# Kernel optimization log

Measured on AMD Instinct MI355X. Metric: run time of the kernel, lower is better.

## Reference

```python
import jax, jax.numpy as jnp
import numpy as np

D_MODEL, WIN, STRIDE, NHEAD, HEAD_DIM, FFN_H = 96, 16, 8, 6, 16, 192
INNER = NHEAD * HEAD_DIM
EPS = 1e-5


def _ln(x, g, b):
    m = jnp.mean(x, axis=-1, keepdims=True)
    v = jnp.mean((x - m) ** 2, axis=-1, keepdims=True)
    return (x - m) / jnp.sqrt(v + EPS) * g + b


def setup_inputs() -> dict:
    key = jax.random.key(0)
    ks = jax.random.split(key, 16)
    B, L, D = 32, 8192, D_MODEL
    sd = lambda n: 1.0 / np.sqrt(n)
    return {
        "x": jax.random.normal(ks[0], (B, L, D), jnp.float32),
        "ln1_g": jnp.ones((D,), jnp.float32),
        "ln1_b": jnp.zeros((D,), jnp.float32),
        "qkv_w": jax.random.normal(ks[1], (D, 3 * INNER), jnp.float32) * sd(D),
        "qkv_b": jnp.zeros((3 * INNER,), jnp.float32),
        "out_w": jax.random.normal(ks[2], (INNER, D), jnp.float32) * sd(INNER),
        "out_b": jnp.zeros((D,), jnp.float32),
        "ln2_g": jnp.ones((D,), jnp.float32),
        "ln2_b": jnp.zeros((D,), jnp.float32),
        "ffn_w1": jax.random.normal(ks[3], (D, FFN_H), jnp.float32) * sd(D),
        "ffn_b1": jnp.zeros((FFN_H,), jnp.float32),
        "ffn_w2": jax.random.normal(ks[4], (FFN_H, D), jnp.float32) * sd(FFN_H),
        "ffn_b2": jnp.zeros((D,), jnp.float32),
        "pln_g": jnp.ones((D,), jnp.float32),
        "pln_b": jnp.zeros((D,), jnp.float32),
    }


def reference(x, ln1_g, ln1_b, qkv_w, qkv_b, out_w, out_b,
              ln2_g, ln2_b, ffn_w1, ffn_b1, ffn_w2, ffn_b2, pln_g, pln_b):
    B, L, D = x.shape
    w, s = WIN, STRIDE
    num_win = 1 + (L - w) // s  # all windows fit since (num_win-1)*s + w <= L
    idx = jnp.arange(num_win)[:, None] * s + jnp.arange(w)[None, :]  # [N, w]

    seg = x[:, idx]  # [B, N, w, D] gather of overlapping windows

    # --- pre-LN attention block, vectorized over all windows ---
    h = _ln(seg, ln1_g, ln1_b)
    qkv = h @ qkv_w + qkv_b  # [B, N, w, 3*INNER]
    q, k, v = jnp.split(qkv, 3, axis=-1)
    shp = (B, num_win, w, NHEAD, HEAD_DIM)
    q, k, v = q.reshape(shp), k.reshape(shp), v.reshape(shp)
    scores = jnp.einsum('bnqhd,bnkhd->bnhqk', q, k) / np.sqrt(HEAD_DIM).astype(np.float32)
    causal = jnp.tril(jnp.ones((w, w), bool))
    scores = jnp.where(causal, scores, -jnp.inf)
    attn = jax.nn.softmax(scores, axis=-1)
    o = jnp.einsum('bnhqk,bnkhd->bnqhd', attn, v).reshape(B, num_win, w, INNER)
    o = o @ out_w + out_b
    h = seg + o

    # --- FFN block ---
    h2 = _ln(h, ln2_g, ln2_b)
    h = h + (jax.nn.gelu(h2 @ ffn_w1 + ffn_b1) @ ffn_w2 + ffn_b2)
    h = _ln(h, pln_g, pln_b)

    # --- overlap-add average ---
    out = jnp.zeros((B, L, D), x.dtype).at[:, idx].add(h)
    cnt = jnp.zeros((L,), x.dtype).at[idx.reshape(-1)].add(1.0)
    return out / jnp.maximum(cnt, 1.0)[None, :, None]
```

## Files before the change

### kernel.cpp

```cpp
#include <hip/hip_runtime.h>
#include <hip/hip_bf16.h>

typedef __attribute__((ext_vector_type(8))) short short8;
typedef __attribute__((ext_vector_type(4))) float f32x4;
typedef __attribute__((ext_vector_type(4))) unsigned u32x4;

#define LDS_BYTES 40960
#define SH   104
#define SU   52
#define KOFF 3328
#define VOFF 6656
#define F1S  200
#define F1SU 100

#if __has_builtin(__builtin_amdgcn_cvt_pk_bf16_f32)
typedef __attribute__((ext_vector_type(2))) __bf16 bf16x2;
__device__ __forceinline__ unsigned pk2bf(float a, float b){
  bf16x2 v = __builtin_amdgcn_cvt_pk_bf16_f32(a, b);
  return __builtin_bit_cast(unsigned, v);
}
__device__ __forceinline__ unsigned short f2bf(float x){
  bf16x2 v = __builtin_amdgcn_cvt_pk_bf16_f32(x, x);
  return (unsigned short)(__builtin_bit_cast(unsigned, v) & 0xFFFFu);
}
#else
__device__ __forceinline__ unsigned short f2bf(float x){
  unsigned u = __float_as_uint(x);
  u += 0x7FFFu + ((u >> 16) & 1u);
  return (unsigned short)(u >> 16);
}
__device__ __forceinline__ unsigned pk2bf(float a, float b){
  return (unsigned)f2bf(a) | ((unsigned)f2bf(b) << 16);
}
#endif

#if __has_builtin(__builtin_amdgcn_rcpf)
__device__ __forceinline__ float fast_rcp(float x){ return __builtin_amdgcn_rcpf(x); }
#else
__device__ __forceinline__ float fast_rcp(float x){ return 1.f/x; }
#endif
#if __has_builtin(__builtin_amdgcn_rsqf)
__device__ __forceinline__ float fast_rsq(float x){ return __builtin_amdgcn_rsqf(x); }
#else
__device__ __forceinline__ float fast_rsq(float x){ return rsqrtf(x); }
#endif
#if __has_builtin(__builtin_amdgcn_exp2f)
__device__ __forceinline__ float fast_ex2(float x){ return __builtin_amdgcn_exp2f(x); }
#else
__device__ __forceinline__ float fast_ex2(float x){ return exp2f(x); }
#endif

__device__ __forceinline__ float bflo(unsigned u){ return __uint_as_float(u << 16); }
__device__ __forceinline__ float bfhi(unsigned u){ return __uint_as_float(u & 0xFFFF0000u); }
__device__ __forceinline__ float bf1(unsigned short h){ return __uint_as_float(((unsigned)h) << 16); }

__global__ void zero_stripes(float* __restrict__ out){
  int k = blockIdx.x;
  int b = blockIdx.y;
  int t = threadIdx.x;
  int tok = 24*k + (t / 24);
  f32x4 z = {0.f, 0.f, 0.f, 0.f};
  *(f32x4*)(out + ((size_t)b*8192 + tok)*96 + 4*(t % 24)) = z;
}

__global__ void pack_weights(const float* __restrict__ qkv_w, const float* __restrict__ out_w,
                             const float* __restrict__ ffn_w1, const float* __restrict__ ffn_w2,
                             short8* __restrict__ wsv){
  int f = blockIdx.x, lane = threadIdx.x;
  const float* W; int N, nt, kf;
  if (f < 54)      { W = qkv_w;  N = 288; nt = f/3;        kf = f%3; }
  else if (f < 72) { int i=f-54;  W = out_w;  N = 96;  nt = i/3; kf = i%3; }
  else if (f < 108){ int i=f-72;  W = ffn_w1; N = 192; nt = i/3; kf = i%3; }
  else             { int i=f-108; W = ffn_w2; N = 96;  nt = i/6; kf = i%6; }
  int n = lane & 15, kq = lane >> 4;
  short8 v;
#pragma unroll
  for (int j = 0; j < 8; ++j){
    int k = kf*32 + kq*8 + j;
    v[j] = (short)f2bf(W[(size_t)k * N + nt*16 + n]);
  }
  wsv[f*64 + lane] = v;
}

__global__ __launch_bounds__(512, 8)
void fused_block(const float* __restrict__ x,
                 const float* __restrict__ ln1_g, const float* __restrict__ ln1_b,
                 const float* __restrict__ qkv_b,
                 const float* __restrict__ out_b,
                 const float* __restrict__ ln2_g, const float* __restrict__ ln2_b,
                 const float* __restrict__ ffn_b1, const float* __restrict__ ffn_b2,
                 const float* __restrict__ pln_g, const float* __restrict__ pln_b,
                 const short8* __restrict__ wsv,
                 float* __restrict__ out)
{
  __shared__ __align__(16) char smem[LDS_BYTES];
  unsigned short* hres  = (unsigned short*)smem;
  unsigned*       hresU = (unsigned*)smem;
  unsigned short* buf1  = (unsigned short*)(smem + 9984);
  unsigned*       buf1U = (unsigned*)(smem + 9984);
  unsigned short* buf2  = (unsigned short*)(smem + 19968);
  unsigned*       buf2U = (unsigned*)(smem + 19968);

  const int tid  = threadIdx.x;
  const int wave = tid >> 6, lane = tid & 63;
  const int lm   = lane & 15, quad = lane >> 4;
  __builtin_assume(wave >= 0 && wave < 8);
  __builtin_assume(lm >= 0 && lm < 16);
  __builtin_assume(quad >= 0 && quad < 4);
  const int g = blockIdx.x, b = blockIdx.y;
  const int t0 = 24 * g;
  const size_t xbase = ((size_t)b * 8192 + t0) * 96;
  const short8* wl = wsv + lane;

  {
    const int row = tid >> 4, j = tid & 15;
    const float* xr = x + xbase + (size_t)row*96 + 6*j;
    float v[6];
#pragma unroll
    for (int e = 0; e < 3; ++e){ float2 t = *(const float2*)(xr + 2*e); v[2*e]=t.x; v[2*e+1]=t.y; }
    float s = 0.f, q2 = 0.f;
#pragma unroll
    for (int e = 0; e < 6; ++e){ s += v[e]; q2 += v[e]*v[e]; }
#pragma unroll
    for (int m = 1; m < 16; m <<= 1){ s += __shfl_xor(s, m, 16); q2 += __shfl_xor(q2, m, 16); }
    float mean = s * (1.f/96.f);
    float rstd = fast_rsq(q2 * (1.f/96.f) - mean*mean + 1e-5f);
#pragma unroll
    for (int e = 0; e < 3; ++e){
      float2 gg = *(const float2*)(ln1_g + 6*j + 2*e);
      float2 bb = *(const float2*)(ln1_b + 6*j + 2*e);
      buf1U[row*SU + 3*j + e] = pk2bf((v[2*e]-mean)*rstd*gg.x+bb.x,
                                      (v[2*e+1]-mean)*rstd*gg.y+bb.y);
    }
  }
  __syncthreads();

  {
    const int mt = wave & 1, p = wave >> 1;
    __builtin_assume(p >= 0 && p < 4);
    const unsigned short* arow = buf1 + (16*mt + lm)*SH + quad*8;
    short8 h0 = *(const short8*)(arow);
    short8 h1 = *(const short8*)(arow + 32);
    short8 h2 = *(const short8*)(arow + 64);
    auto qkv_tile = [&](int nt){
      if (nt < 12){
        f32x4 acc0 = *(const f32x4*)(qkv_b + nt*16 + quad*4);
        f32x4 acc1 = {0.f,0.f,0.f,0.f};
        acc0 = __builtin_amdgcn_mfma_f32_16x16x32_bf16(wl[(nt*3+0)*64], h0, acc0, 0, 0, 0);
        acc1 = __builtin_amdgcn_mfma_f32_16x16x32_bf16(wl[(nt*3+1)*64], h1, acc1, 0, 0, 0);
        acc0 = __builtin_amdgcn_mfma_f32_16x16x32_bf16(wl[(nt*3+2)*64], h2, acc0, 0, 0, 0);
        int row = 16*mt + lm;
        unsigned idx = (nt < 6)
          ? (unsigned)(row*SU + nt*8 + quad*2)
          : (unsigned)((KOFF>>1) + row*SU + (nt-6)*8 + quad*2);
        buf2U[idx]     = pk2bf(acc0[0]+acc1[0], acc0[1]+acc1[1]);
        buf2U[idx + 1] = pk2bf(acc0[2]+acc1[2], acc0[3]+acc1[3]);
      } else {
        int col = nt*16 + lm;
        float bias = qkv_b[col];
        f32x4 acc0 = {bias, bias, bias, bias};
        f32x4 acc1 = {0.f,0.f,0.f,0.f};
        acc0 = __builtin_amdgcn_mfma_f32_16x16x32_bf16(h0, wl[(nt*3+0)*64], acc0, 0, 0, 0);
        acc1 = __builtin_amdgcn_mfma_f32_16x16x32_bf16(h1, wl[(nt*3+1)*64], acc1, 0, 0, 0);
        acc0 = __builtin_amdgcn_mfma_f32_16x16x32_bf16(h2, wl[(nt*3+2)*64], acc0, 0, 0, 0);
        int d2 = col - 192;
        int w0 = (VOFF >> 1) + d2*20 + 8*mt + 2*quad;
        buf2U[w0]     = pk2bf(acc0[0]+acc1[0], acc0[1]+acc1[1]);
        buf2U[w0 + 1] = pk2bf(acc0[2]+acc1[2], acc0[3]+acc1[3]);
      }
    };
#pragma unroll
    for (int i = 0; i < 4; ++i) qkv_tile(p + 4*i);
    if (p < 2) qkv_tile(p + 16);
  }
  __syncthreads();

  {
    const short8 z8 = {0,0,0,0,0,0,0,0};
    short8 qa0=z8,ka0=z8,va0=z8, qa1=z8,ka1=z8,va1=z8, qa2=z8,ka2=z8,va2=z8;
    const int u0 = wave, u1 = wave + 8, u2 = wave + 16;
    const int w0_=u0/6, h0_=u0-6*(u0/6), w1_=u1/6, h1_=u1-6*(u1/6);
    const int w2_=u2/6, h2_=u2-6*(u2/6);
    if (quad < 2){
      qa0 = *(const short8*)(buf2 +        (8*w0_ + lm)*SH + h0_*16 + quad*8);
      ka0 = *(const short8*)(buf2 + KOFF + (8*w0_ + lm)*SH + h0_*16 + quad*8);
      va0 = *(const short8*)(buf2 + VOFF + (h0_*16 + lm)*40 + 8*w0_ + quad*8);
      qa1 = *(const short8*)(buf2 +        (8*w1_ + lm)*SH + h1_*16 + quad*8);
      ka1 = *(const short8*)(buf2 + KOFF + (8*w1_ + lm)*SH + h1_*16 + quad*8);
      va1 = *(const short8*)(buf2 + VOFF + (h1_*16 + lm)*40 + 8*w1_ + quad*8);
      if (wave < 2){
        qa2 = *(const short8*)(buf2 +        (8*w2_ + lm)*SH + h2_*16 + quad*8);
        ka2 = *(const short8*)(buf2 + KOFF + (8*w2_ + lm)*SH + h2_*16 + quad*8);
        va2 = *(const short8*)(buf2 + VOFF + (h2_*16 + lm)*40 + 8*w2_ + quad*8);
      }
    }
    auto attn_compute = [&](short8 qa, short8 ka, short8 va, int w, int h){
      f32x4 sc = {0.f,0.f,0.f,0.f};
      sc = __builtin_amdgcn_mfma_f32_16x16x32_bf16(ka, qa, sc, 0, 0, 0);
      float p4[4]; float sum = 0.f;
#pragma unroll
      for (int r = 0; r < 4; ++r){
        int k = quad*4 + r;
        float e = fast_ex2(sc[r]*0.36067376f);
        p4[r] = (k <= lm) ? e : 0.f;
        sum += p4[r];
      }
      sum += __shfl_xor(sum, 16);
      sum += __shfl_xor(sum, 32);
      float rs = fast_rcp(sum);
      int x0 = (int)pk2bf(p4[0]*rs, p4[1]*rs);
      int x1 = (int)pk2bf(p4[2]*rs, p4[3]*rs);
      int srcA = lm + ((quad & 1) << 5);
      int e0 = __shfl(x0, srcA),      e1 = __shfl(x1, srcA);
      int e2 = __shfl(x0, srcA + 16), e3 = __shfl(x1, srcA + 16);
      short8 pa = z8;
      if (quad < 2){
        u32x4 t = {(unsigned)e0, (unsigned)e1, (unsigned)e2, (unsigned)e3};
        pa = __builtin_bit_cast(short8, t);
      }
      f32x4 oc = {0.f,0.f,0.f,0.f};
      oc = __builtin_amdgcn_mfma_f32_16x16x32_bf16(va, pa, oc, 0, 0, 0);
      unsigned ob = (w*16 + lm)*SU + h*8 + quad*2;
      buf1U[ob]     = pk2bf(oc[0], oc[1]);
      buf1U[ob + 1] = pk2bf(oc[2], oc[3]);
    };
    attn_compute(qa0, ka0, va0, w0_, h0_);
    attn_compute(qa1, ka1, va1, w1_, h1_);
    if (wave < 2) attn_compute(qa2, ka2, va2, w2_, h2_);
  }
  __syncthreads();

  if (wave < 6){
    const int w = wave >> 1, ntb = (wave & 1)*3;
    const unsigned short* arow = buf1 + (w*16 + lm)*SH + quad*8;
    short8 a0 = *(const short8*)(arow);
    short8 a1 = *(const short8*)(arow + 32);
    short8 a2 = *(const short8*)(arow + 64);
    f32x4 xr[3];
#pragma unroll
    for (int i = 0; i < 3; ++i)
      xr[i] = *(const f32x4*)(x + xbase + (size_t)(8*w + lm)*96 + (ntb+i)*16 + quad*4);
#pragma unroll
    for (int i = 0; i < 3; ++i){
      int nt = ntb + i;
      f32x4 acc0 = *(const f32x4*)(out_b + nt*16 + quad*4);
      f32x4 acc1 = {0.f,0.f,0.f,0.f};
      acc0 = __builtin_amdgcn_mfma_f32_16x16x32_bf16(wl[(54 + nt*3 + 0)*64], a0, acc0, 0, 0, 0);
      acc1 = __builtin_amdgcn_mfma_f32_16x16x32_bf16(wl[(54 + nt*3 + 1)*64], a1, acc1, 0, 0, 0);
      acc0 = __builtin_amdgcn_mfma_f32_16x16x32_bf16(wl[(54 + nt*3 + 2)*64], a2, acc0, 0, 0, 0);
      unsigned idx = (w*16 + lm)*SU + nt*8 + quad*2;
      hresU[idx]     = pk2bf(acc0[0]+acc1[0]+xr[i][0], acc0[1]+acc1[1]+xr[i][1]);
      hresU[idx + 1] = pk2bf(acc0[2]+acc1[2]+xr[i][2], acc0[3]+acc1[3]+xr[i][3]);
    }
  }
  __syncthreads();

  {
    const int j = tid & 15;
#pragma unroll
    for (int p = 0; p < 2; ++p){
      int row = p*32 + (tid >> 4);
      if (row < 48){
        float v[6];
#pragma unroll
        for (int e = 0; e < 3; ++e){
          unsigned u = hresU[row*SU + 3*j + e];
          v[2*e] = bflo(u); v[2*e+1] = bfhi(u);
        }
        float s = 0.f, q2 = 0.f;
#pragma unroll
        for (int e = 0; e < 6; ++e){ s += v[e]; q2 += v[e]*v[e]; }
#pragma unroll
        for (int m = 1; m < 16; m <<= 1){ s += __shfl_xor(s, m, 16); q2 += __shfl_xor(q2, m, 16); }
        float mean = s * (1.f/96.f);
        float rstd = fast_rsq(q2 * (1.f/96.f) - mean*mean + 1e-5f);
#pragma unroll
        for (int e = 0; e < 3; ++e){
          float2 gg = *(const float2*)(ln2_g + 6*j + 2*e);
          float2 bb = *(const float2*)(ln2_b + 6*j + 2*e);
          buf1U[row*SU + 3*j + e] = pk2bf((v[2*e]-mean)*rstd*gg.x+bb.x,
                                          (v[2*e+1]-mean)*rstd*gg.y+bb.y);
        }
      }
    }
  }
  __syncthreads();

  if (wave < 6){
    const int mt = wave >> 1, ntb = (wave & 1)*6;
    const unsigned short* arow = buf1 + (mt*16 + lm)*SH + quad*8;
    short8 a0 = *(const short8*)(arow);
    short8 a1 = *(const short8*)(arow + 32);
    short8 a2 = *(const short8*)(arow + 64);
#pragma unroll
    for (int i = 0; i < 6; ++i){
      int nt = ntb + i;
      f32x4 acc0 = *(const f32x4*)(ffn_b1 + nt*16 + quad*4);
      f32x4 acc1 = {0.f,0.f,0.f,0.f};
      acc0 = __builtin_amdgcn_mfma_f32_16x16x32_bf16(wl[(72 + nt*3 + 0)*64], a0, acc0, 0, 0, 0);
      acc1 = __builtin_amdgcn_mfma_f32_16x16x32_bf16(wl[(72 + nt*3 + 1)*64], a1, acc1, 0, 0, 0);
      acc0 = __builtin_amdgcn_mfma_f32_16x16x32_bf16(wl[(72 + nt*3 + 2)*64], a2, acc0, 0, 0, 0);
      float gl[4];
#pragma unroll
      for (int r = 0; r < 4; ++r){
        float uu = acc0[r] + acc1[r];
        float z = -2.3022081f * (uu + 0.044715f * uu*uu*uu);
        float e = fast_ex2(z);
        gl[r] = uu * fast_rcp(1.f + e);
      }
      unsigned idx = (mt*16 + lm)*F1SU + nt*8 + quad*2;
      buf2U[idx]     = pk2bf(gl[0], gl[1]);
      buf2U[idx + 1] = pk2bf(gl[2], gl[3]);
    }
  }
  __syncthreads();

  if (wave < 6){
    const int mt = wave >> 1, ntb = (wave & 1)*3;
    const unsigned short* frow = buf2 + (mt*16 + lm)*F1S + quad*8;
    short8 f0 = *(const short8*)(frow);
    short8 f1 = *(const short8*)(frow + 32);
    short8 f2 = *(const short8*)(frow + 64);
    short8 f3 = *(const short8*)(frow + 96);
    short8 f4 = *(const short8*)(frow + 128);
    short8 f5 = *(const short8*)(frow + 160);
#pragma unroll
    for (int i = 0; i < 3; ++i){
      int nt = ntb + i;
      f32x4 acc0 = *(const f32x4*)(ffn_b2 + nt*16 + quad*4);
      f32x4 acc1 = {0.f,0.f,0.f,0.f};
      acc0 = __builtin_amdgcn_mfma_f32_16x16x32_bf16(wl[(108 + nt*6 + 0)*64], f0, acc0, 0, 0, 0);
      acc1 = __builtin_amdgcn_mfma_f32_16x16x32_bf16(wl[(108 + nt*6 + 1)*64], f1, acc1, 0, 0, 0);
      acc0 = __builtin_amdgcn_mfma_f32_16x16x32_bf16(wl[(108 + nt*6 + 2)*64], f2, acc0, 0, 0, 0);
      acc1 = __builtin_amdgcn_mfma_f32_16x16x32_bf16(wl[(108 + nt*6 + 3)*64], f3, acc1, 0, 0, 0);
      acc0 = __builtin_amdgcn_mfma_f32_16x16x32_bf16(wl[(108 + nt*6 + 4)*64], f4, acc0, 0, 0, 0);
      acc1 = __builtin_amdgcn_mfma_f32_16x16x32_bf16(wl[(108 + nt*6 + 5)*64], f5, acc1, 0, 0, 0);
      unsigned idx = (mt*16 + lm)*SU + nt*8 + quad*2;
      unsigned u0 = hresU[idx], u1 = hresU[idx + 1];
      hresU[idx]     = pk2bf(bflo(u0)+acc0[0]+acc1[0], bfhi(u0)+acc0[1]+acc1[1]);
      hresU[idx + 1] = pk2bf(bflo(u1)+acc0[2]+acc1[2], bfhi(u1)+acc0[3]+acc1[3]);
    }
  }
  __syncthreads();

  {
    const int i = tid >> 4, c0 = tid & 15;
    const int l = t0 + i;
    const size_t obase = ((size_t)b * 8192 + l) * 96;
    int rowA, rowB = -1;
    if (i < 8)       rowA = i;
    else if (i < 16){ rowA = i;            rowB = 16 + (i - 8); }
    else if (i < 24){ rowA = 16 + (i - 8); rowB = 32 + (i - 16); }
    else             rowA = 32 + (i - 16);

    float g6[6], b6[6];
#pragma unroll
    for (int e = 0; e < 6; ++e){ g6[e] = pln_g[c0 + 16*e]; b6[e] = pln_b[c0 + 16*e]; }

    float yA[6];
    {
      float v[6];
#pragma unroll
      for (int e = 0; e < 6; ++e) v[e] = bf1(hres[rowA*SH + c0 + 16*e]);
      float s = 0.f, q2 = 0.f;
#pragma unroll
      for (int e = 0; e < 6; ++e){ s += v[e]; q2 += v[e]*v[e]; }
#pragma unroll
      for (int m = 1; m < 16; m <<= 1){ s += __shfl_xor(s, m, 16); q2 += __shfl_xor(q2, m, 16); }
      float mean = s * (1.f/96.f);
      float rstd = fast_rsq(q2 * (1.f/96.f) - mean*mean + 1e-5f);
#pragma unroll
      for (int e = 0; e < 6; ++e) yA[e] = (v[e]-mean)*rstd*g6[e] + b6[e];
    }
    if (rowB >= 0){
      float yB[6];
      {
        float v[6];
#pragma unroll
        for (int e = 0; e < 6; ++e) v[e] = bf1(hres[rowB*SH + c0 + 16*e]);
        float s = 0.f, q2 = 0.f;
#pragma unroll
        for (int e = 0; e < 6; ++e){ s += v[e]; q2 += v[e]*v[e]; }
#pragma unroll
        for (int m = 1; m < 16; m <<= 1){ s += __shfl_xor(s, m, 16); q2 += __shfl_xor(q2, m, 16); }
        float mean = s * (1.f/96.f);
        float rstd = fast_rsq(q2 * (1.f/96.f) - mean*mean + 1e-5f);
#pragma unroll
        for (int e = 0; e < 6; ++e) yB[e] = (v[e]-mean)*rstd*g6[e] + b6[e];
      }
#pragma unroll
      for (int e = 0; e < 6; ++e)
        out[obase + c0 + 16*e] = 0.5f * (yA[e] + yB[e]);
    } else {
      float inv = (l < 8 || l >= 8184) ? 1.0f : 0.5f;
#pragma unroll
      for (int e = 0; e < 6; ++e)
        atomicAdd(&out[obase + c0 + 16*e], yA[e] * inv);
    }
  }
}

extern "C" void kernel_launch(void* const* d_in, const int* in_sizes, int n_in,
                              void* d_out, int out_size, void* d_ws, size_t ws_size,
                              hipStream_t stream) {
  const float* x      = (const float*)d_in[0];
  const float* ln1_g  = (const float*)d_in[1];
  const float* ln1_b  = (const float*)d_in[2];
  const float* qkv_w  = (const float*)d_in[3];
  const float* qkv_b  = (const float*)d_in[4];
  const float* out_w  = (const float*)d_in[5];
  const float* out_b  = (const float*)d_in[6];
  const float* ln2_g  = (const float*)d_in[7];
  const float* ln2_b  = (const float*)d_in[8];
  const float* ffn_w1 = (const float*)d_in[9];
  const float* ffn_b1 = (const float*)d_in[10];
  const float* ffn_w2 = (const float*)d_in[11];
  const float* ffn_b2 = (const float*)d_in[12];
  const float* pln_g  = (const float*)d_in[13];
  const float* pln_b  = (const float*)d_in[14];
  float* out = (float*)d_out;
  short8* wsv = (short8*)d_ws;

  zero_stripes<<<dim3(342, 32), 192, 0, stream>>>(out);
  pack_weights<<<144, 64, 0, stream>>>(qkv_w, out_w, ffn_w1, ffn_w2, wsv);
  fused_block<<<dim3(341, 32), 512, 0, stream>>>(
      x, ln1_g, ln1_b, qkv_b, out_b, ln2_g, ln2_b, ffn_b1, ffn_b2,
      pln_g, pln_b, (const short8*)wsv, out);
}
```

Baseline: 449.6 us.

## Fuse LayerNorms into MFMA fragment loads and rebalance GEMM tiles across all waves

```diff
diff --git a/kernel.cpp b/kernel.cpp
--- a/kernel.cpp
+++ b/kernel.cpp
@@ -113,35 +113,52 @@
   const short8* wl = wsv + lane;
 
   {
-    const int row = tid >> 4, j = tid & 15;
-    const float* xr = x + xbase + (size_t)row*96 + 6*j;
-    float v[6];
-#pragma unroll
-    for (int e = 0; e < 3; ++e){ float2 t = *(const float2*)(xr + 2*e); v[2*e]=t.x; v[2*e+1]=t.y; }
+    const int mt = wave & 1, p = wave >> 1;
+    __builtin_assume(p >= 0 && p < 4);
+    const int row = 16*mt + lm;
+    const float* xr = x + xbase + (size_t)row*96 + quad*8;
+    float v0[8], v1[8], v2[8];
+    {
+      f32x4 a = *(const f32x4*)(xr);       f32x4 c = *(const f32x4*)(xr + 4);
+#pragma unroll
+      for (int j = 0; j < 4; ++j){ v0[j] = a[j]; v0[4+j] = c[j]; }
+    }
+    {
+      f32x4 a = *(const f32x4*)(xr + 32);  f32x4 c = *(const f32x4*)(xr + 36);
+#pragma unroll
+      for (int j = 0; j < 4; ++j){ v1[j] = a[j]; v1[4+j] = c[j]; }
+    }
+    {
+      f32x4 a = *(const f32x4*)(xr + 64);  f32x4 c = *(const f32x4*)(xr + 68);
+#pragma unroll
+      for (int j = 0; j < 4; ++j){ v2[j] = a[j]; v2[4+j] = c[j]; }
+    }
     float s = 0.f, q2 = 0.f;
 #pragma unroll
-    for (int e = 0; e < 6; ++e){ s += v[e]; q2 += v[e]*v[e]; }
-#pragma unroll
-    for (int m = 1; m < 16; m <<= 1){ s += __shfl_xor(s, m, 16); q2 += __shfl_xor(q2, m, 16); }
+    for (int j = 0; j < 8; ++j){
+      s += v0[j] + v1[j] + v2[j];
+      q2 += v0[j]*v0[j] + v1[j]*v1[j] + v2[j]*v2[j];
+    }
+    s  += __shfl_xor(s, 16);  q2 += __shfl_xor(q2, 16);
+    s  += __shfl_xor(s, 32);  q2 += __shfl_xor(q2, 32);
     float mean = s * (1.f/96.f);
     float rstd = fast_rsq(q2 * (1.f/96.f) - mean*mean + 1e-5f);
-#pragma unroll
-    for (int e = 0; e < 3; ++e){
-      float2 gg = *(const float2*)(ln1_g + 6*j + 2*e);
-      float2 bb = *(const float2*)(ln1_b + 6*j + 2*e);
-      buf1U[row*SU + 3*j + e] = pk2bf((v[2*e]-mean)*rstd*gg.x+bb.x,
-                                      (v[2*e+1]-mean)*rstd*gg.y+bb.y);
-    }
-  }
-  __syncthreads();
-
-  {
-    const int mt = wave & 1, p = wave >> 1;
-    __builtin_assume(p >= 0 && p < 4);
-    const unsigned short* arow = buf1 + (16*mt + lm)*SH + quad*8;
-    short8 h0 = *(const short8*)(arow);
-    short8 h1 = *(const short8*)(arow + 32);
-    short8 h2 = *(const short8*)(arow + 64);
+
+    short8 h0, h1, h2;
+    auto mkfrag = [&](const float* vv, int kf)->short8{
+      const float* gp = ln1_g + kf*32 + quad*8;
+      const float* bp = ln1_b + kf*32 + quad*8;
+      f32x4 ga = *(const f32x4*)(gp), gb = *(const f32x4*)(gp + 4);
+      f32x4 ba = *(const f32x4*)(bp), bb = *(const f32x4*)(bp + 4);
+      u32x4 hu;
+      hu[0] = pk2bf((vv[0]-mean)*rstd*ga[0]+ba[0], (vv[1]-mean)*rstd*ga[1]+ba[1]);
+      hu[1] = pk2bf((vv[2]-mean)*rstd*ga[2]+ba[2], (vv[3]-mean)*rstd*ga[3]+ba[3]);
+      hu[2] = pk2bf((vv[4]-mean)*rstd*gb[0]+bb[0], (vv[5]-mean)*rstd*gb[1]+bb[1]);
+      hu[3] = pk2bf((vv[6]-mean)*rstd*gb[2]+bb[2], (vv[7]-mean)*rstd*gb[3]+bb[3]);
+      return __builtin_bit_cast(short8, hu);
+    };
+    h0 = mkfrag(v0, 0); h1 = mkfrag(v1, 1); h2 = mkfrag(v2, 2);
+
     auto qkv_tile = [&](int nt){
       if (nt < 12){
         f32x4 acc0 = *(const f32x4*)(qkv_b + nt*16 + quad*4);
@@ -149,7 +166,6 @@
         acc0 = __builtin_amdgcn_mfma_f32_16x16x32_bf16(wl[(nt*3+0)*64], h0, acc0, 0, 0, 0);
         acc1 = __builtin_amdgcn_mfma_f32_16x16x32_bf16(wl[(nt*3+1)*64], h1, acc1, 0, 0, 0);
         acc0 = __builtin_amdgcn_mfma_f32_16x16x32_bf16(wl[(nt*3+2)*64], h2, acc0, 0, 0, 0);
-        int row = 16*mt + lm;
         unsigned idx = (nt < 6)
           ? (unsigned)(row*SU + nt*8 + quad*2)
           : (unsigned)((KOFF>>1) + row*SU + (nt-6)*8 + quad*2);
@@ -176,25 +192,13 @@
   __syncthreads();
 
   {
-    const short8 z8 = {0,0,0,0,0,0,0,0};
-    short8 qa0=z8,ka0=z8,va0=z8, qa1=z8,ka1=z8,va1=z8, qa2=z8,ka2=z8,va2=z8;
-    const int u0 = wave, u1 = wave + 8, u2 = wave + 16;
-    const int w0_=u0/6, h0_=u0-6*(u0/6), w1_=u1/6, h1_=u1-6*(u1/6);
-    const int w2_=u2/6, h2_=u2-6*(u2/6);
-    if (quad < 2){
-      qa0 = *(const short8*)(buf2 +        (8*w0_ + lm)*SH + h0_*16 + quad*8);
-      ka0 = *(const short8*)(buf2 + KOFF + (8*w0_ + lm)*SH + h0_*16 + quad*8);
-      va0 = *(const short8*)(buf2 + VOFF + (h0_*16 + lm)*40 + 8*w0_ + quad*8);
-      qa1 = *(const short8*)(buf2 +        (8*w1_ + lm)*SH + h1_*16 + quad*8);
-      ka1 = *(const short8*)(buf2 + KOFF + (8*w1_ + lm)*SH + h1_*16 + quad*8);
-      va1 = *(const short8*)(buf2 + VOFF + (h1_*16 + lm)*40 + 8*w1_ + quad*8);
-      if (wave < 2){
-        qa2 = *(const short8*)(buf2 +        (8*w2_ + lm)*SH + h2_*16 + quad*8);
-        ka2 = *(const short8*)(buf2 + KOFF + (8*w2_ + lm)*SH + h2_*16 + quad*8);
-        va2 = *(const short8*)(buf2 + VOFF + (h2_*16 + lm)*40 + 8*w2_ + quad*8);
-      }
-    }
-    auto attn_compute = [&](short8 qa, short8 ka, short8 va, int w, int h){
+    auto attn_unit = [&](int u){
+      int w = u / 6, h = u - 6*(u / 6);
+      short8 qa = {0,0,0,0,0,0,0,0}, ka = {0,0,0,0,0,0,0,0};
+      if (quad < 2){
+        qa = *(const short8*)(buf2 +        (8*w + lm)*SH + h*16 + quad*8);
+        ka = *(const short8*)(buf2 + KOFF + (8*w + lm)*SH + h*16 + quad*8);
+      }
       f32x4 sc = {0.f,0.f,0.f,0.f};
       sc = __builtin_amdgcn_mfma_f32_16x16x32_bf16(ka, qa, sc, 0, 0, 0);
       float p4[4]; float sum = 0.f;
@@ -213,10 +217,11 @@
       int srcA = lm + ((quad & 1) << 5);
       int e0 = __shfl(x0, srcA),      e1 = __shfl(x1, srcA);
       int e2 = __shfl(x0, srcA + 16), e3 = __shfl(x1, srcA + 16);
-      short8 pa = z8;
+      short8 pa = {0,0,0,0,0,0,0,0}, va = {0,0,0,0,0,0,0,0};
       if (quad < 2){
         u32x4 t = {(unsigned)e0, (unsigned)e1, (unsigned)e2, (unsigned)e3};
         pa = __builtin_bit_cast(short8, t);
+        va = *(const short8*)(buf2 + VOFF + (h*16 + lm)*40 + 8*w + quad*8);
       }
       f32x4 oc = {0.f,0.f,0.f,0.f};
       oc = __builtin_amdgcn_mfma_f32_16x16x32_bf16(va, pa, oc, 0, 0, 0);
@@ -224,82 +229,82 @@
       buf1U[ob]     = pk2bf(oc[0], oc[1]);
       buf1U[ob + 1] = pk2bf(oc[2], oc[3]);
     };
-    attn_compute(qa0, ka0, va0, w0_, h0_);
-    attn_compute(qa1, ka1, va1, w1_, h1_);
-    if (wave < 2) attn_compute(qa2, ka2, va2, w2_, h2_);
+    attn_unit(wave);
+    attn_unit(wave + 8);
+    if (wave < 2) attn_unit(wave + 16);
   }
   __syncthreads();
 
-  if (wave < 6){
-    const int w = wave >> 1, ntb = (wave & 1)*3;
-    const unsigned short* arow = buf1 + (w*16 + lm)*SH + quad*8;
-    short8 a0 = *(const short8*)(arow);
-    short8 a1 = *(const short8*)(arow + 32);
-    short8 a2 = *(const short8*)(arow + 64);
-    f32x4 xr[3];
-#pragma unroll
-    for (int i = 0; i < 3; ++i)
-      xr[i] = *(const f32x4*)(x + xbase + (size_t)(8*w + lm)*96 + (ntb+i)*16 + quad*4);
-#pragma unroll
-    for (int i = 0; i < 3; ++i){
-      int nt = ntb + i;
+  {
+    auto oproj_tile = [&](int tile){
+      int w = tile / 6, nt = tile - 6*(tile / 6);
       f32x4 acc0 = *(const f32x4*)(out_b + nt*16 + quad*4);
       f32x4 acc1 = {0.f,0.f,0.f,0.f};
+      const unsigned short* arow = buf1 + (w*16 + lm)*SH + quad*8;
+      short8 a0 = *(const short8*)(arow);
+      short8 a1 = *(const short8*)(arow + 32);
+      short8 a2 = *(const short8*)(arow + 64);
       acc0 = __builtin_amdgcn_mfma_f32_16x16x32_bf16(wl[(54 + nt*3 + 0)*64], a0, acc0, 0, 0, 0);
       acc1 = __builtin_amdgcn_mfma_f32_16x16x32_bf16(wl[(54 + nt*3 + 1)*64], a1, acc1, 0, 0, 0);
       acc0 = __builtin_amdgcn_mfma_f32_16x16x32_bf16(wl[(54 + nt*3 + 2)*64], a2, acc0, 0, 0, 0);
+      f32x4 xr = *(const f32x4*)(x + xbase + (size_t)(8*w + lm)*96 + nt*16 + quad*4);
       unsigned idx = (w*16 + lm)*SU + nt*8 + quad*2;
-      hresU[idx]     = pk2bf(acc0[0]+acc1[0]+xr[i][0], acc0[1]+acc1[1]+xr[i][1]);
-      hresU[idx + 1] = pk2bf(acc0[2]+acc1[2]+xr[i][2], acc0[3]+acc1[3]+xr[i][3]);
-    }
-  }
-  __syncthreads();
-
-  {
-    const int j = tid & 15;
-#pragma unroll
-    for (int p = 0; p < 2; ++p){
-      int row = p*32 + (tid >> 4);
-      if (row < 48){
-        float v[6];
-#pragma unroll
-        for (int e = 0; e < 3; ++e){
-          unsigned u = hresU[row*SU + 3*j + e];
-          v[2*e] = bflo(u); v[2*e+1] = bfhi(u);
-        }
-        float s = 0.f, q2 = 0.f;
-#pragma unroll
-        for (int e = 0; e < 6; ++e){ s += v[e]; q2 += v[e]*v[e]; }
-#pragma unroll
-        for (int m = 1; m < 16; m <<= 1){ s += __shfl_xor(s, m, 16); q2 += __shfl_xor(q2, m, 16); }
-        float mean = s * (1.f/96.f);
-        float rstd = fast_rsq(q2 * (1.f/96.f) - mean*mean + 1e-5f);
-#pragma unroll
-        for (int e = 0; e < 3; ++e){
-          float2 gg = *(const float2*)(ln2_g + 6*j + 2*e);
-          float2 bb = *(const float2*)(ln2_b + 6*j + 2*e);
-          buf1U[row*SU + 3*j + e] = pk2bf((v[2*e]-mean)*rstd*gg.x+bb.x,
-                                          (v[2*e+1]-mean)*rstd*gg.y+bb.y);
-        }
-      }
-    }
+      hresU[idx]     = pk2bf(acc0[0]+acc1[0]+xr[0], acc0[1]+acc1[1]+xr[1]);
+      hresU[idx + 1] = pk2bf(acc0[2]+acc1[2]+xr[2], acc0[3]+acc1[3]+xr[3]);
+    };
+    oproj_tile(wave);
+    oproj_tile(wave + 8);
+    if (wave < 2) oproj_tile(wave + 16);
   }
   __syncthreads();
 
   if (wave < 6){
     const int mt = wave >> 1, ntb = (wave & 1)*6;
-    const unsigned short* arow = buf1 + (mt*16 + lm)*SH + quad*8;
-    short8 a0 = *(const short8*)(arow);
-    short8 a1 = *(const short8*)(arow + 32);
-    short8 a2 = *(const short8*)(arow + 64);
+    const int row = 16*mt + lm;
+    const unsigned short* hr = hres + row*SH + quad*8;
+    short8 r0 = *(const short8*)(hr);
+    short8 r1 = *(const short8*)(hr + 32);
+    short8 r2 = *(const short8*)(hr + 64);
+    u32x4 c0 = __builtin_bit_cast(u32x4, r0);
+    u32x4 c1 = __builtin_bit_cast(u32x4, r1);
+    u32x4 c2 = __builtin_bit_cast(u32x4, r2);
+    float s = 0.f, q2 = 0.f;
+#pragma unroll
+    for (int t = 0; t < 4; ++t){
+      float a0 = bflo(c0[t]), a1 = bfhi(c0[t]);
+      float a2 = bflo(c1[t]), a3 = bfhi(c1[t]);
+      float a4 = bflo(c2[t]), a5 = bfhi(c2[t]);
+      s  += a0+a1+a2+a3+a4+a5;
+      q2 += a0*a0+a1*a1+a2*a2+a3*a3+a4*a4+a5*a5;
+    }
+    s  += __shfl_xor(s, 16);  q2 += __shfl_xor(q2, 16);
+    s  += __shfl_xor(s, 32);  q2 += __shfl_xor(q2, 32);
+    float mean = s * (1.f/96.f);
+    float rstd = fast_rsq(q2 * (1.f/96.f) - mean*mean + 1e-5f);
+
+    short8 a0f, a1f, a2f;
+    auto mkfrag2 = [&](u32x4 c, int kf)->short8{
+      const float* gp = ln2_g + kf*32 + quad*8;
+      const float* bp = ln2_b + kf*32 + quad*8;
+      f32x4 ga = *(const f32x4*)(gp), gb = *(const f32x4*)(gp + 4);
+      f32x4 ba = *(const f32x4*)(bp), bb = *(const f32x4*)(bp + 4);
+      u32x4 hu;
+      hu[0] = pk2bf((bflo(c[0])-mean)*rstd*ga[0]+ba[0], (bfhi(c[0])-mean)*rstd*ga[1]+ba[1]);
+      hu[1] = pk2bf((bflo(c[1])-mean)*rstd*ga[2]+ba[2], (bfhi(c[1])-mean)*rstd*ga[3]+ba[3]);
+      hu[2] = pk2bf((bflo(c[2])-mean)*rstd*gb[0]+bb[0], (bfhi(c[2])-mean)*rstd*gb[1]+bb[1]);
+      hu[3] = pk2bf((bflo(c[3])-mean)*rstd*gb[2]+bb[2], (bfhi(c[3])-mean)*rstd*gb[3]+bb[3]);
+      return __builtin_bit_cast(short8, hu);
+    };
+    a0f = mkfrag2(c0, 0); a1f = mkfrag2(c1, 1); a2f = mkfrag2(c2, 2);
+
 #pragma unroll
     for (int i = 0; i < 6; ++i){
       int nt = ntb + i;
       f32x4 acc0 = *(const f32x4*)(ffn_b1 + nt*16 + quad*4);
       f32x4 acc1 = {0.f,0.f,0.f,0.f};
-      acc0 = __builtin_amdgcn_mfma_f32_16x16x32_bf16(wl[(72 + nt*3 + 0)*64], a0, acc0, 0, 0, 0);
-      acc1 = __builtin_amdgcn_mfma_f32_16x16x32_bf16(wl[(72 + nt*3 + 1)*64], a1, acc1, 0, 0, 0);
-      acc0 = __builtin_amdgcn_mfma_f32_16x16x32_bf16(wl[(72 + nt*3 + 2)*64], a2, acc0, 0, 0, 0);
+      acc0 = __builtin_amdgcn_mfma_f32_16x16x32_bf16(wl[(72 + nt*3 + 0)*64], a0f, acc0, 0, 0, 0);
+      acc1 = __builtin_amdgcn_mfma_f32_16x16x32_bf16(wl[(72 + nt*3 + 1)*64], a1f, acc1, 0, 0, 0);
+      acc0 = __builtin_amdgcn_mfma_f32_16x16x32_bf16(wl[(72 + nt*3 + 2)*64], a2f, acc0, 0, 0, 0);
       float gl[4];
 #pragma unroll
       for (int r = 0; r < 4; ++r){
@@ -315,18 +320,16 @@
   }
   __syncthreads();
 
-  if (wave < 6){
-    const int mt = wave >> 1, ntb = (wave & 1)*3;
-    const unsigned short* frow = buf2 + (mt*16 + lm)*F1S + quad*8;
-    short8 f0 = *(const short8*)(frow);
-    short8 f1 = *(const short8*)(frow + 32);
-    short8 f2 = *(const short8*)(frow + 64);
-    short8 f3 = *(const short8*)(frow + 96);
-    short8 f4 = *(const short8*)(frow + 128);
-    short8 f5 = *(const short8*)(frow + 160);
-#pragma unroll
-    for (int i = 0; i < 3; ++i){
-      int nt = ntb + i;
+  {
+    auto ffn2_tile = [&](int tile){
+      int mt = tile / 6, nt = tile - 6*(tile / 6);
+      const unsigned short* frow = buf2 + (mt*16 + lm)*F1S + quad*8;
+      short8 f0 = *(const short8*)(frow);
+      short8 f1 = *(const short8*)(frow + 32);
+      short8 f2 = *(const short8*)(frow + 64);
+      short8 f3 = *(const short8*)(frow + 96);
+      short8 f4 = *(const short8*)(frow + 128);
+      short8 f5 = *(const short8*)(frow + 160);
       f32x4 acc0 = *(const f32x4*)(ffn_b2 + nt*16 + quad*4);
       f32x4 acc1 = {0.f,0.f,0.f,0.f};
       acc0 = __builtin_amdgcn_mfma_f32_16x16x32_bf16(wl[(108 + nt*6 + 0)*64], f0, acc0, 0, 0, 0);
@@ -339,7 +342,10 @@
       unsigned u0 = hresU[idx], u1 = hresU[idx + 1];
       hresU[idx]     = pk2bf(bflo(u0)+acc0[0]+acc1[0], bfhi(u0)+acc0[1]+acc1[1]);
       hresU[idx + 1] = pk2bf(bflo(u1)+acc0[2]+acc1[2], bfhi(u1)+acc0[3]+acc1[3]);
-    }
+    };
+    ffn2_tile(wave);
+    ffn2_tile(wave + 8);
+    if (wave < 2) ffn2_tile(wave + 16);
   }
   __syncthreads();
 
```

After: 510.2 us. 13.5% more time.
